# Optimization experiments

Measured on AMD Instinct MI355X. Metric: run time of the kernel, lower is better.

## Reference

```python
import jax, jax.numpy as jnp
import numpy as np

M, N = 4096, 4096

def _make_expk(n):
    k = np.arange(n, dtype=np.float64) * np.pi / (2.0 * n)
    return jnp.asarray(np.stack([np.cos(k), np.sin(k)], axis=-1), dtype=jnp.float32)

def setup_inputs() -> dict:
    key = jax.random.key(0)
    x = jax.random.normal(key, (M, N), dtype=jnp.float32)
    return {"x": x, "expkM": _make_expk(M), "expkN": _make_expk(N)}

def _idct_last(X, expk):
    """1D IDCT (inverse of unnormalized DCT-II) along last axis via Makhoul's
    N-point FFT trick. expk[k] = (cos, sin) of pi*k/(2N), i.e. e^{j pi k/(2N)}."""
    n = X.shape[-1]
    Xv = X * 0.5
    # V[k] = (Xv[k] - j*Xv[n-k]) * e^{j pi k/(2n)}, with imag part 0 at k=0
    tail = -jnp.flip(Xv, axis=-1)[..., :-1]
    Vi = jnp.concatenate([jnp.zeros_like(Xv[..., :1]), tail], axis=-1)
    W = expk[:, 0] + 1j * expk[:, 1]
    V = (Xv + 1j * Vi) * W
    v = jnp.fft.ifft(V, axis=-1).real.astype(X.dtype)
    # de-interleave: out[2m] = v[m], out[2m+1] = v[n-1-m]
    out = jnp.zeros_like(X)
    out = out.at[..., 0::2].set(v[..., : n - n // 2])
    out = out.at[..., 1::2].set(jnp.flip(v, axis=-1)[..., : n // 2])
    return out

def reference(x, expkM, expkN):
    # separable 2D IDCT: last axis (N) then first axis (M)
    y = _idct_last(x, expkN)
    y = _idct_last(y.T, expkM).T
    return y
```

## Files before the change

kernel.cpp:

```cpp
#include <hip/hip_runtime.h>
#include <math.h>


#define TT 256

constexpr float W64R[32] = {
    1.0f, 0.995184726672197f, 0.980785280403230f, 0.956940335732209f,
    0.923879532511287f, 0.881921264348355f, 0.831469612302545f, 0.773010453362737f,
    0.707106781186548f, 0.634393284163645f, 0.555570233019602f, 0.471396736825998f,
    0.382683432365090f, 0.290284677254462f, 0.195090322016128f, 0.0980171403295606f,
    0.0f, -0.0980171403295606f, -0.195090322016128f, -0.290284677254462f,
    -0.382683432365090f, -0.471396736825998f, -0.555570233019602f, -0.634393284163645f,
    -0.707106781186548f, -0.773010453362737f, -0.831469612302545f, -0.881921264348355f,
    -0.923879532511287f, -0.956940335732209f, -0.980785280403230f, -0.995184726672197f};
constexpr float W64I[32] = {
    0.0f, 0.0980171403295606f, 0.195090322016128f, 0.290284677254462f,
    0.382683432365090f, 0.471396736825998f, 0.555570233019602f, 0.634393284163645f,
    0.707106781186548f, 0.773010453362737f, 0.831469612302545f, 0.881921264348355f,
    0.923879532511287f, 0.956940335732209f, 0.980785280403230f, 0.995184726672197f,
    1.0f, 0.995184726672197f, 0.980785280403230f, 0.956940335732209f,
    0.923879532511287f, 0.881921264348355f, 0.831469612302545f, 0.773010453362737f,
    0.707106781186548f, 0.634393284163645f, 0.555570233019602f, 0.471396736825998f,
    0.382683432365090f, 0.290284677254462f, 0.195090322016128f, 0.0980171403295606f};

__device__ __forceinline__ constexpr int brev(int x, int bits) {
    int r = 0;
    for (int i = 0; i < bits; ++i) { r = (r << 1) | (x & 1); x >>= 1; }
    return r;
}

__device__ __forceinline__ float vadd(float a, float b) { return a + b; }
__device__ __forceinline__ float vsub(float a, float b) { return a - b; }
__device__ __forceinline__ float vmul(float a, float s) { return a * s; }
__device__ __forceinline__ float2 vadd(float2 a, float2 b) { return make_float2(a.x + b.x, a.y + b.y); }
__device__ __forceinline__ float2 vsub(float2 a, float2 b) { return make_float2(a.x - b.x, a.y - b.y); }
__device__ __forceinline__ float2 vmul(float2 a, float s) { return make_float2(a.x * s, a.y * s); }

template <int NP, typename V>
__device__ __forceinline__ void fft_dif(V* re, V* im) {
#pragma unroll
    for (int h = NP / 2; h >= 1; h >>= 1) {
#pragma unroll
        for (int b = 0; b < NP; b += 2 * h) {
#pragma unroll
            for (int k = 0; k < h; ++k) {
                V ur = re[b + k], ui = im[b + k];
                V vr = re[b + k + h], vi = im[b + k + h];
                V dr = vsub(ur, vr), di = vsub(ui, vi);
                re[b + k] = vadd(ur, vr);
                im[b + k] = vadd(ui, vi);
                float wr = W64R[k * (32 / h)], wi = W64I[k * (32 / h)];
                re[b + k + h] = vsub(vmul(dr, wr), vmul(di, wi));
                im[b + k + h] = vadd(vmul(dr, wi), vmul(di, wr));
            }
        }
    }
}

__global__ void tw_init_kernel(float2* __restrict__ tw2048,
                               float2* __restrict__ ca, float2* __restrict__ cb,
                               float2* __restrict__ cc, float2* __restrict__ cd) {
    int k = blockIdx.x * TT + threadIdx.x;
    const double s = 0.5 / 4096.0;
    double aw = M_PI * (double)k / 2048.0;
    double wr = cos(aw), wi = sin(aw);
    double a1 = M_PI * (double)k / 8192.0;
    double e1r = cos(a1), e1i = sin(a1);
    double a2 = M_PI * (double)(k + 2048) / 8192.0;
    double e2r = cos(a2), e2i = sin(a2);
    double Ar = s * ((1.0 - wi) * e1r - wr * e1i);
    double Ai = s * ((1.0 - wi) * e1i + wr * e1r);
    double Br = (k == 0) ? 0.0 : Ai;
    double Bi = (k == 0) ? 0.0 : -Ar;
    double Cr = s * ((1.0 + wi) * e2r + wr * e2i);
    double Ci = s * ((1.0 + wi) * e2i - wr * e2r);
    ca[k] = make_float2((float)Ar, (float)Ai);
    cb[k] = make_float2((float)Br, (float)Bi);
    cc[k] = make_float2((float)Cr, (float)Ci);
    cd[k] = make_float2((float)Ci, (float)-Cr);
    double at = M_PI * (double)k / 1024.0;
    tw2048[k] = make_float2((float)cos(at), (float)sin(at));
}

__global__ __launch_bounds__(TT) void col_a_kernel(
    const float* __restrict__ x,
    const float2* __restrict__ ca, const float2* __restrict__ cb,
    const float2* __restrict__ cc, const float2* __restrict__ cd,
    const float2* __restrict__ tw2048, float2* __restrict__ T1) {
    int c2 = blockIdx.x * 64 + threadIdx.x;
    int k1 = blockIdx.y * 4 + threadIdx.y;
    const float2* __restrict__ xv = (const float2*)x;
    float2 fr[32], fi[32];
#pragma unroll
    for (int k2 = 0; k2 < 32; ++k2) {
        int k = k1 + 64 * k2;
        float2 xa = xv[(size_t)k * 2048 + c2];
        float2 xb = xv[(size_t)((4096 - k) & 4095) * 2048 + c2];
        float2 xc = xv[(size_t)(2048 + k) * 2048 + c2];
        float2 xd = xv[(size_t)(2048 - k) * 2048 + c2];
        float2 A = ca[k], B = cb[k], C = cc[k], D = cd[k];
        fr[k2] = make_float2(A.x * xa.x + B.x * xb.x + C.x * xc.x + D.x * xd.x,
                             A.x * xa.y + B.x * xb.y + C.x * xc.y + D.x * xd.y);
        fi[k2] = make_float2(A.y * xa.x + B.y * xb.x + C.y * xc.x + D.y * xd.x,
                             A.y * xa.y + B.y * xb.y + C.y * xc.y + D.y * xd.y);
    }
    fft_dif<32, float2>(fr, fi);
#pragma unroll
    for (int j = 0; j < 32; ++j) {
        int n2 = brev(j, 5);
        float2 w = tw2048[k1 * n2];
        float2 orr = vsub(vmul(fr[j], w.x), vmul(fi[j], w.y));
        float2 oii = vadd(vmul(fr[j], w.y), vmul(fi[j], w.x));
        float4 o = make_float4(orr.x, oii.x, orr.y, oii.y);
        *(float4*)&T1[(size_t)(k1 * 32 + n2) * 4096 + 2 * c2] = o;
    }
}

__global__ __launch_bounds__(TT) void col_b_kernel(
    const float2* __restrict__ T1, float* __restrict__ out) {
    __shared__ float L[128 * 68];
    int tx = threadIdx.x, ty = threadIdx.y;
    int c = blockIdx.x * 64 + tx;
    int n2 = blockIdx.y * 4 + ty;
    float re[64], im[64];
#pragma unroll
    for (int k1 = 0; k1 < 64; ++k1) {
        float2 v = T1[(size_t)(k1 * 32 + n2) * 4096 + c];
        re[k1] = v.x; im[k1] = v.y;
    }
    fft_dif<64, float>(re, im);
    int tlin = ty * 64 + tx;
#pragma unroll
    for (int g = 0; g < 4; ++g) {
        if (ty == g) {
#pragma unroll
            for (int j = 0; j < 64; ++j) {
                int n1 = brev(j, 6);
                L[(2 * n1) * 68 + tx] = re[j];
                L[(2 * n1 + 1) * 68 + tx] = im[j];
            }
        }
        __syncthreads();
        int n2g = blockIdx.y * 4 + g;
#pragma unroll
        for (int u = 0; u < 8; ++u) {
            int idx = tlin + 256 * u;
            int slot = idx >> 4, xp = idx & 15;
            int n1 = slot >> 1;
            int m = 32 * n1 + n2g;
            int row = (n1 < 32) ? (4 * m + ((slot & 1) ? 2 : 0))
                                : (((slot & 1) ? 8189 : 8191) - 4 * m);
            float4 v = *(const float4*)&L[slot * 68 + 4 * xp];
            *(float4*)&out[(size_t)row * 4096 + blockIdx.x * 64 + 4 * xp] = v;
        }
        __syncthreads();
    }
}

#define C_SQ2 0.70710678118654752440f
__device__ __forceinline__ void radix8(const float* ar, const float* ai,
                                       float* tr, float* ti) {
    float s04r = ar[0] + ar[4], s04i = ai[0] + ai[4];
    float d04r = ar[0] - ar[4], d04i = ai[0] - ai[4];
    float s26r = ar[2] + ar[6], s26i = ai[2] + ai[6];
    float d26r = ar[2] - ar[6], d26i = ai[2] - ai[6];
    float E0r = s04r + s26r, E0i = s04i + s26i;
    float E1r = d04r - d26i, E1i = d04i + d26r;
    float E2r = s04r - s26r, E2i = s04i - s26i;
    float E3r = d04r + d26i, E3i = d04i - d26r;
    float s15r = ar[1] + ar[5], s15i = ai[1] + ai[5];
    float d15r = ar[1] - ar[5], d15i = ai[1] - ai[5];
    float s37r = ar[3] + ar[7], s37i = ai[3] + ai[7];
    float d37r = ar[3] - ar[7], d37i = ai[3] - ai[7];
    float O0r = s15r + s37r, O0i = s15i + s37i;
    float O1r = d15r - d37i, O1i = d15i + d37r;
    float O2r = s15r - s37r, O2i = s15i - s37i;
    float O3r = d15r + d37i, O3i = d15i - d37r;
    float W1r = C_SQ2 * (O1r - O1i), W1i = C_SQ2 * (O1r + O1i);
    float W2r = -O2i, W2i = O2r;
    float W3r = -C_SQ2 * (O3r + O3i), W3i = C_SQ2 * (O3r - O3i);
    tr[0] = E0r + O0r; ti[0] = E0i + O0i;
    tr[4] = E0r - O0r; ti[4] = E0i - O0i;
    tr[1] = E1r + W1r; ti[1] = E1i + W1i;
    tr[5] = E1r - W1r; ti[5] = E1i - W1i;
    tr[2] = E2r + W2r; ti[2] = E2i + W2i;
    tr[6] = E2r - W2r; ti[6] = E2i - W2i;
    tr[3] = E3r + W3r; ti[3] = E3i + W3i;
    tr[7] = E3r - W3r; ti[7] = E3i - W3i;
}

__global__ __launch_bounds__(TT) void idct_rows_kernel(
    const float2* __restrict__ ca, const float2* __restrict__ cb,
    const float2* __restrict__ cc, const float2* __restrict__ cd,
    const float2* __restrict__ tw2048, float* __restrict__ io) {
    __shared__ float pool[8576];
    float* b0r = pool;
    float* b0i = pool + 2112;
    float* b1r = pool + 4224;
    float* b1i = pool + 6400;
    float* stg = pool + 4224;
    const int t = threadIdx.x;
    float* __restrict__ xr = io + (size_t)blockIdx.x * 4096;

#pragma unroll
    for (int u = 0; u < 4; ++u) {
        int idx = t + 256 * u;
        float4 v = ((const float4*)xr)[idx];
        *(float4*)&stg[4 * idx] = v;
    }
    __syncthreads();

    float zr[8], zi[8], tr[8], ti[8];
#pragma unroll
    for (int p = 0; p < 8; ++p) {
        int k = t + 256 * p;
        float xa = stg[k];
        float xb = stg[(4096 - k) & 4095];
        float xc = stg[2048 + k];
        float xd = stg[2048 - k];
        float2 A = ca[k], B = cb[k], C = cc[k], D = cd[k];
        zr[p] = A.x * xa + B.x * xb + C.x * xc + D.x * xd;
        zi[p] = A.y * xa + B.y * xb + C.y * xc + D.y * xd;
    }
    radix8(zr, zi, tr, ti);
    {
        int baseA = 8 * t + (t >> 2);
        b0r[baseA] = tr[0]; b0i[baseA] = ti[0];
#pragma unroll
        for (int q = 1; q < 8; ++q) {
            float2 w = tw2048[(t * q) & 2047];
            b0r[baseA + q] = w.x * tr[q] - w.y * ti[q];
            b0i[baseA + q] = w.x * ti[q] + w.y * tr[q];
        }
    }
    __syncthreads();
    {
        float ar[8], ai[8];
        int rb = t + (t >> 5);
#pragma unroll
        for (int p = 0; p < 8; ++p) { ar[p] = b0r[rb + 264 * p]; ai[p] = b0i[rb + 264 * p]; }
        radix8(ar, ai, tr, ti);
        int j = t >> 3, k = t & 7, wj = 8 * j;
        int baseB = 68 * j + k;
        b1r[baseB] = tr[0]; b1i[baseB] = ti[0];
#pragma unroll
        for (int q = 1; q < 8; ++q) {
            int off = baseB + 8 * q + (q >> 1);
            float2 w = tw2048[(wj * q) & 2047];
            b1r[off] = w.x * tr[q] - w.y * ti[q];
            b1i[off] = w.x * ti[q] + w.y * tr[q];
        }
    }
    __syncthreads();
    {
        float ar[8], ai[8];
        int rb = t + (t >> 4);
#pragma unroll
        for (int p = 0; p < 8; ++p) { ar[p] = b1r[rb + 272 * p]; ai[p] = b1i[rb + 272 * p]; }
        radix8(ar, ai, tr, ti);
        int j = t >> 6, wj = 64 * j, k = t & 63;
        int baseC = 528 * j + k + (k >> 5);
        b0r[baseC] = tr[0]; b0i[baseC] = ti[0];
#pragma unroll
        for (int q = 1; q < 8; ++q) {
            int off = baseC + 66 * q;
            float2 w = tw2048[(wj * q) & 2047];
            b0r[off] = w.x * tr[q] - w.y * ti[q];
            b0i[off] = w.x * ti[q] + w.y * tr[q];
        }
    }
    __syncthreads();
#pragma unroll
    for (int u = 0; u < 2; ++u) {
        int b = t + 256 * u;
        int rb = b + (b >> 5);
        int wb = b + (b >> 4);
        float a0r = b0r[rb], a0i = b0i[rb];
        float a1r = b0r[rb + 528], a1i = b0i[rb + 528];
        float a2r = b0r[rb + 1056], a2i = b0i[rb + 1056];
        float a3r = b0r[rb + 1584], a3i = b0i[rb + 1584];
        float s02r = a0r + a2r, s02i = a0i + a2i;
        float d02r = a0r - a2r, d02i = a0i - a2i;
        float s13r = a1r + a3r, s13i = a1i + a3i;
        float d13r = a1r - a3r, d13i = a1i - a3i;
        b1r[wb] = s02r + s13r;          b1i[wb] = s02i + s13i;
        b1r[wb + 544] = d02r - d13i;    b1i[wb + 544] = d02i + d13r;
        b1r[wb + 1088] = s02r - s13r;   b1i[wb + 1088] = s02i - s13i;
        b1r[wb + 1632] = d02r + d13i;   b1i[wb + 1632] = d02i - d13r;
    }
    __syncthreads();
#pragma unroll
    for (int i = 0; i < 4; ++i) {
        int s = t + 256 * i;
        int l2 = 2047 - s;
        int ms = s + (s >> 4);
        int ml = l2 + (l2 >> 4);
        float4 o = make_float4(b1r[ms], b1i[ml], b1i[ms], b1r[ml]);
        *(float4*)&xr[4 * s] = o;
    }
}

extern "C" void kernel_launch(void* const* d_in, const int* in_sizes, int n_in,
                              void* d_out, int out_size, void* d_ws, size_t ws_size,
                              hipStream_t stream) {
    const float* x = (const float*)d_in[0];
    float* out = (float*)d_out;

    float2* tw2048 = (float2*)d_ws;
    float2* ca = (float2*)((char*)d_ws + 1 * 16384);
    float2* cb = (float2*)((char*)d_ws + 2 * 16384);
    float2* cc = (float2*)((char*)d_ws + 3 * 16384);
    float2* cd = (float2*)((char*)d_ws + 4 * 16384);
    float2* T1 = (float2*)((char*)d_ws + (1 << 20));

    tw_init_kernel<<<8, TT, 0, stream>>>(tw2048, ca, cb, cc, cd);
    col_a_kernel<<<dim3(32, 16), dim3(64, 4), 0, stream>>>(x, ca, cb, cc, cd, tw2048, T1);
    col_b_kernel<<<dim3(64, 8), dim3(64, 4), 0, stream>>>(T1, out);
    idct_rows_kernel<<<4096, TT, 0, stream>>>(ca, cb, cc, cd, tw2048, out);
}
```

Before: 199.6 us.

## Stage column-pass global loads through double-buffered LDS with wide float4 reads

Both column kernels now fetch their input with coalesced float4 loads into a double-buffered shared-memory stage, prefetching the next chunk while the current one is consumed. col_a is remapped to one k1 per block covering 256 columns with one scalar column per thread, and caches the mixing coefficients and per-row twiddles in LDS. The aim is to replace scattered per-thread strided global loads with wide contiguous transactions and to overlap load latency with compute. In exchange there are more __syncthreads barriers and more shared memory per block, which could lower occupancy.

```diff
diff --git a/kernel.cpp b/kernel.cpp
--- a/kernel.cpp
+++ b/kernel.cpp
@@ -29,29 +29,22 @@
     return r;
 }
 
-__device__ __forceinline__ float vadd(float a, float b) { return a + b; }
-__device__ __forceinline__ float vsub(float a, float b) { return a - b; }
-__device__ __forceinline__ float vmul(float a, float s) { return a * s; }
-__device__ __forceinline__ float2 vadd(float2 a, float2 b) { return make_float2(a.x + b.x, a.y + b.y); }
-__device__ __forceinline__ float2 vsub(float2 a, float2 b) { return make_float2(a.x - b.x, a.y - b.y); }
-__device__ __forceinline__ float2 vmul(float2 a, float s) { return make_float2(a.x * s, a.y * s); }
-
-template <int NP, typename V>
-__device__ __forceinline__ void fft_dif(V* re, V* im) {
+template <int NP>
+__device__ __forceinline__ void fft_dif(float* re, float* im) {
 #pragma unroll
     for (int h = NP / 2; h >= 1; h >>= 1) {
 #pragma unroll
         for (int b = 0; b < NP; b += 2 * h) {
 #pragma unroll
             for (int k = 0; k < h; ++k) {
-                V ur = re[b + k], ui = im[b + k];
-                V vr = re[b + k + h], vi = im[b + k + h];
-                V dr = vsub(ur, vr), di = vsub(ui, vi);
-                re[b + k] = vadd(ur, vr);
-                im[b + k] = vadd(ui, vi);
+                float ur = re[b + k], ui = im[b + k];
+                float vr = re[b + k + h], vi = im[b + k + h];
+                float dr = ur - vr, di = ui - vi;
+                re[b + k] = ur + vr;
+                im[b + k] = ui + vi;
                 float wr = W64R[k * (32 / h)], wi = W64I[k * (32 / h)];
-                re[b + k + h] = vsub(vmul(dr, wr), vmul(di, wi));
-                im[b + k + h] = vadd(vmul(dr, wi), vmul(di, wr));
+                re[b + k + h] = dr * wr - di * wi;
+                im[b + k + h] = dr * wi + di * wr;
             }
         }
     }
@@ -87,49 +80,141 @@
     const float2* __restrict__ ca, const float2* __restrict__ cb,
     const float2* __restrict__ cc, const float2* __restrict__ cd,
     const float2* __restrict__ tw2048, float2* __restrict__ T1) {
-    int c2 = blockIdx.x * 64 + threadIdx.x;
-    int k1 = blockIdx.y * 4 + threadIdx.y;
-    const float2* __restrict__ xv = (const float2*)x;
-    float2 fr[32], fi[32];
-#pragma unroll
-    for (int k2 = 0; k2 < 32; ++k2) {
+    __shared__ float stage[8192];
+    __shared__ float2 coefs[32][4];
+    __shared__ float2 twn[32];
+    const int tid = threadIdx.x;
+    const int k1 = blockIdx.y;
+    const int cbase = blockIdx.x * 256;
+
+    if (tid < 128) {
+        int k2 = tid >> 2, src = tid & 3;
         int k = k1 + 64 * k2;
-        float2 xa = xv[(size_t)k * 2048 + c2];
-        float2 xb = xv[(size_t)((4096 - k) & 4095) * 2048 + c2];
-        float2 xc = xv[(size_t)(2048 + k) * 2048 + c2];
-        float2 xd = xv[(size_t)(2048 - k) * 2048 + c2];
-        float2 A = ca[k], B = cb[k], C = cc[k], D = cd[k];
-        fr[k2] = make_float2(A.x * xa.x + B.x * xb.x + C.x * xc.x + D.x * xd.x,
-                             A.x * xa.y + B.x * xb.y + C.x * xc.y + D.x * xd.y);
-        fi[k2] = make_float2(A.y * xa.x + B.y * xb.x + C.y * xc.x + D.y * xd.x,
-                             A.y * xa.y + B.y * xb.y + C.y * xc.y + D.y * xd.y);
-    }
-    fft_dif<32, float2>(fr, fi);
+        const float2* tbl = (src == 0) ? ca : (src == 1) ? cb : (src == 2) ? cc : cd;
+        coefs[k2][src] = tbl[k];
+    } else if (tid < 160) {
+        int n2 = tid - 128;
+        twn[n2] = tw2048[(k1 * n2) & 2047];
+    }
+
+    const int f4l = tid & 63;
+    const int segw = tid >> 6;
+
+    auto gaddr = [&](int ch, int r) -> const float4* {
+        int seg = r * 4 + segw;
+        int src = seg & 3, k2l = seg >> 2;
+        int k = k1 + 64 * (4 * ch + k2l);
+        int row = (src == 0) ? k
+                : (src == 1) ? ((4096 - k) & 4095)
+                : (src == 2) ? (2048 + k) : (2048 - k);
+        return (const float4*)(x + (size_t)row * 4096 + cbase) + f4l;
+    };
+    auto ldsoff = [&](int buf, int r) -> int {
+        int seg = r * 4 + segw;
+        return buf * 4096 + seg * 256 + 4 * f4l;
+    };
+
+    float4 v[4];
+#pragma unroll
+    for (int r = 0; r < 4; ++r) v[r] = *gaddr(0, r);
+#pragma unroll
+    for (int r = 0; r < 4; ++r) *(float4*)&stage[ldsoff(0, r)] = v[r];
+    __syncthreads();
+
+    float fr[32], fi[32];
+#pragma unroll
+    for (int ch = 0; ch < 8; ++ch) {
+        float4 vn[4];
+        if (ch < 7) {
+#pragma unroll
+            for (int r = 0; r < 4; ++r) vn[r] = *gaddr(ch + 1, r);
+        }
+        const int sb = (ch & 1) * 4096;
+#pragma unroll
+        for (int k2l = 0; k2l < 4; ++k2l) {
+            float xa = stage[sb + (k2l * 4 + 0) * 256 + tid];
+            float xb = stage[sb + (k2l * 4 + 1) * 256 + tid];
+            float xc = stage[sb + (k2l * 4 + 2) * 256 + tid];
+            float xd = stage[sb + (k2l * 4 + 3) * 256 + tid];
+            int k2 = 4 * ch + k2l;
+            float2 A = coefs[k2][0], B = coefs[k2][1];
+            float2 C = coefs[k2][2], D = coefs[k2][3];
+            fr[k2] = A.x * xa + B.x * xb + C.x * xc + D.x * xd;
+            fi[k2] = A.y * xa + B.y * xb + C.y * xc + D.y * xd;
+        }
+        if (ch < 7) {
+#pragma unroll
+            for (int r = 0; r < 4; ++r) *(float4*)&stage[ldsoff((ch + 1) & 1, r)] = vn[r];
+        }
+        __syncthreads();
+    }
+
+    fft_dif<32>(fr, fi);
 #pragma unroll
     for (int j = 0; j < 32; ++j) {
         int n2 = brev(j, 5);
-        float2 w = tw2048[k1 * n2];
-        float2 orr = vsub(vmul(fr[j], w.x), vmul(fi[j], w.y));
-        float2 oii = vadd(vmul(fr[j], w.y), vmul(fi[j], w.x));
-        float4 o = make_float4(orr.x, oii.x, orr.y, oii.y);
-        *(float4*)&T1[(size_t)(k1 * 32 + n2) * 4096 + 2 * c2] = o;
+        float2 w = twn[n2];
+        float2 o = make_float2(fr[j] * w.x - fi[j] * w.y,
+                               fr[j] * w.y + fi[j] * w.x);
+        T1[(size_t)(k1 * 32 + n2) * 4096 + cbase + tid] = o;
     }
 }
 
 __global__ __launch_bounds__(TT) void col_b_kernel(
     const float2* __restrict__ T1, float* __restrict__ out) {
-    __shared__ float L[128 * 68];
-    int tx = threadIdx.x, ty = threadIdx.y;
-    int c = blockIdx.x * 64 + tx;
-    int n2 = blockIdx.y * 4 + ty;
+    __shared__ float pool[8704];
+    float2* stage = (float2*)pool;
+    const int tid = threadIdx.x;
+    const int tx = tid & 63, ty = tid >> 6;
+    const int cbase = blockIdx.x * 64;
+    const int n2base = blockIdx.y * 4;
+
+    const int f4l = tid & 31;
+    const int segw = tid >> 5;
+
+    auto gaddr = [&](int ch, int r) -> const float4* {
+        int seg = r * 8 + segw;
+        int n2l = seg & 3, k1l = seg >> 2;
+        int row = (8 * ch + k1l) * 32 + n2base + n2l;
+        return (const float4*)(T1 + (size_t)row * 4096 + cbase) + f4l;
+    };
+    auto ldsidx = [&](int buf, int r) -> int {
+        int seg = r * 8 + segw;
+        return buf * 2048 + seg * 64 + 2 * f4l;
+    };
+
+    float4 v[4];
+#pragma unroll
+    for (int r = 0; r < 4; ++r) v[r] = *gaddr(0, r);
+#pragma unroll
+    for (int r = 0; r < 4; ++r) *(float4*)&stage[ldsidx(0, r)] = v[r];
+    __syncthreads();
+
     float re[64], im[64];
 #pragma unroll
-    for (int k1 = 0; k1 < 64; ++k1) {
-        float2 v = T1[(size_t)(k1 * 32 + n2) * 4096 + c];
-        re[k1] = v.x; im[k1] = v.y;
-    }
-    fft_dif<64, float>(re, im);
-    int tlin = ty * 64 + tx;
+    for (int ch = 0; ch < 8; ++ch) {
+        float4 vn[4];
+        if (ch < 7) {
+#pragma unroll
+            for (int r = 0; r < 4; ++r) vn[r] = *gaddr(ch + 1, r);
+        }
+        const int sb = (ch & 1) * 2048;
+#pragma unroll
+        for (int k1l = 0; k1l < 8; ++k1l) {
+            float2 z = stage[sb + (k1l * 4 + ty) * 64 + tx];
+            re[8 * ch + k1l] = z.x;
+            im[8 * ch + k1l] = z.y;
+        }
+        if (ch < 7) {
+#pragma unroll
+            for (int r = 0; r < 4; ++r) *(float4*)&stage[ldsidx((ch + 1) & 1, r)] = vn[r];
+        }
+        __syncthreads();
+    }
+
+    fft_dif<64>(re, im);
+
+    float* L = pool;
 #pragma unroll
     for (int g = 0; g < 4; ++g) {
         if (ty == g) {
@@ -141,17 +226,17 @@
             }
         }
         __syncthreads();
-        int n2g = blockIdx.y * 4 + g;
+        int n2g = n2base + g;
 #pragma unroll
         for (int u = 0; u < 8; ++u) {
-            int idx = tlin + 256 * u;
+            int idx = tid + 256 * u;
             int slot = idx >> 4, xp = idx & 15;
             int n1 = slot >> 1;
             int m = 32 * n1 + n2g;
             int row = (n1 < 32) ? (4 * m + ((slot & 1) ? 2 : 0))
                                 : (((slot & 1) ? 8189 : 8191) - 4 * m);
-            float4 v = *(const float4*)&L[slot * 68 + 4 * xp];
-            *(float4*)&out[(size_t)row * 4096 + blockIdx.x * 64 + 4 * xp] = v;
+            float4 w = *(const float4*)&L[slot * 68 + 4 * xp];
+            *(float4*)&out[(size_t)row * 4096 + cbase + 4 * xp] = w;
         }
         __syncthreads();
     }
@@ -314,7 +399,7 @@
     float2* T1 = (float2*)((char*)d_ws + (1 << 20));
 
     tw_init_kernel<<<8, TT, 0, stream>>>(tw2048, ca, cb, cc, cd);
-    col_a_kernel<<<dim3(32, 16), dim3(64, 4), 0, stream>>>(x, ca, cb, cc, cd, tw2048, T1);
-    col_b_kernel<<<dim3(64, 8), dim3(64, 4), 0, stream>>>(T1, out);
+    col_a_kernel<<<dim3(16, 64), TT, 0, stream>>>(x, ca, cb, cc, cd, tw2048, T1);
+    col_b_kernel<<<dim3(64, 8), TT, 0, stream>>>(T1, out);
     idct_rows_kernel<<<4096, TT, 0, stream>>>(ca, cb, cc, cd, tw2048, out);
 }
```

New measurement: 261.5 us. 1.31x slower.
